# Optimization experiments

Hardware: AMD Instinct MI355X
Metric: run time of the kernel (lower is better)

The kernel has to match this reference:

```python
import jax, jax.numpy as jnp
import numpy as np

N_NODES = 100000
N_EDGES = 1600000
DIM = 64


def setup_inputs() -> dict:
    key = jax.random.key(0)
    ks = jax.random.split(key, 10)
    return {
        "h_real": jax.random.normal(ks[0], (N_NODES, DIM), dtype=jnp.float32),
        "h_imag": jax.random.normal(ks[1], (N_NODES, DIM), dtype=jnp.float32),
        "d": jax.random.uniform(ks[2], (N_NODES,), dtype=jnp.float32),
        "w_real": jax.random.normal(ks[3], (N_EDGES,), dtype=jnp.float32),
        "w_imag": jax.random.normal(ks[4], (N_EDGES,), dtype=jnp.float32),
        "src": jax.random.randint(ks[5], (N_EDGES,), 0, N_NODES, dtype=jnp.int32),
        "dst": jax.random.randint(ks[6], (N_EDGES,), 0, N_NODES, dtype=jnp.int32),
        "W1": jax.random.normal(ks[7], (DIM, DIM), dtype=jnp.float32) * (1.414 / np.sqrt(DIM)),
        "b1": jnp.zeros((DIM,), dtype=jnp.float32),
        "W2": jax.random.normal(ks[8], (DIM, DIM), dtype=jnp.float32) * (1.414 / np.sqrt(DIM)),
        "b2": jnp.zeros((DIM,), dtype=jnp.float32),
    }


def reference(h_real, h_imag, d, w_real, w_imag, src, dst, W1, b1, W2, b2):
    n = h_real.shape[0]
    # per-edge complex coefficient e = d_dst * d_src * (w_real + i w_imag)
    dd = d[dst] * d[src]                      # [E]
    e_r = (dd * w_real)[:, None]              # [E,1]
    e_i = (dd * w_imag)[:, None]              # [E,1]
    hr = h_real[src]                          # [E,D]
    hi = h_imag[src]                          # [E,D]
    # complex multiply e * h, fused single pass over edges
    m_r = e_r * hr - e_i * hi                 # [E,D]
    m_i = e_i * hr + e_r * hi                 # [E,D]
    z_real = jax.ops.segment_sum(m_r, dst, num_segments=n)  # [N,D]
    z_imag = jax.ops.segment_sum(m_i, dst, num_segments=n)  # [N,D]
    # note: original overwrites z_real first, then z_imag uses the NEW z_real
    zr = (z_real @ W1.T + b1) - (z_imag @ W2.T + b2)
    zi = (zr @ W2.T + b2) + (z_imag @ W1.T + b1)
    return zr, zi
```

## Files before the change

kernel.cpp:

```cpp
#include <hip/hip_runtime.h>
#include <hip/hip_bf16.h>

#define N_NODES 100000
#define N_EDGES 1600000
#define DIM 64

#define TILE 4096
#define B1 ((N_EDGES + TILE - 1) / TILE)
#define K1 ((N_NODES + 255) / 256)
#define NCOUNTS (K1 * B1)
#define SCAN_BLOCK 1024
#define NSB ((NCOUNTS + SCAN_BLOCK - 1) / SCAN_BLOCK)
#define PACKB ((N_NODES * DIM + 255) / 256)
#define PLACE_CAP 4736

typedef __attribute__((ext_vector_type(8))) short bf16x8;
typedef __attribute__((ext_vector_type(4))) float f32x4;

#if defined(__has_builtin)
#if __has_builtin(__builtin_amdgcn_fdot2_f32_bf16)
#define HAVE_DOT2 1
typedef __attribute__((ext_vector_type(2))) __bf16 bf16x2v;
#endif
#endif


__device__ __forceinline__ unsigned pack_bf16x2(float lo, float hi) {
  unsigned ulo = (unsigned)__hip_bfloat16_raw(__float2bfloat16(lo)).x;
  unsigned uhi = (unsigned)__hip_bfloat16_raw(__float2bfloat16(hi)).x;
  return ulo | (uhi << 16);
}
__device__ __forceinline__ float unpack_lo(unsigned u) {
  return __int_as_float((int)(u << 16));
}
__device__ __forceinline__ float unpack_hi(unsigned u) {
  return __int_as_float((int)(u & 0xFFFF0000u));
}
__device__ __forceinline__ unsigned short f2bf(float x) {
  return __hip_bfloat16_raw(__float2bfloat16(x)).x;
}

__global__ __launch_bounds__(256) void setup_fused_kernel(
    const float* __restrict__ h_real, const float* __restrict__ h_imag,
    unsigned* __restrict__ hpack, const float* __restrict__ W1,
    const float* __restrict__ b1, const float* __restrict__ W2,
    const float* __restrict__ b2, unsigned short* __restrict__ At,
    float* __restrict__ cvec, const int* __restrict__ dst,
    int* __restrict__ counts) {
  const int bid = blockIdx.x;
  const int tid = threadIdx.x;
  if (bid < PACKB) {
    const int i = bid * 256 + tid;
    if (i < N_NODES * DIM) hpack[i] = pack_bf16x2(h_real[i], h_imag[i]);
    return;
  }
  if (bid < PACKB + 64) {
    const int idx = (bid - PACKB) * 256 + tid;
    if (idx < 128 * 128) {
      const int n = idx >> 7, k = idx & 127;
      float v;
      if (n < 64) {
        v = (k < 64) ? W1[n * 64 + k] : -W2[n * 64 + (k - 64)];
      } else {
        const int nn = n - 64;
        if (k < 64) {
          float s = 0.0f;
          for (int j = 0; j < 64; ++j) s += W1[j * 64 + k] * W2[nn * 64 + j];
          v = s;
        } else {
          const int kk = k - 64;
          float s = 0.0f;
          for (int j = 0; j < 64; ++j) s += W2[j * 64 + kk] * W2[nn * 64 + j];
          v = W1[nn * 64 + kk] - s;
        }
      }
      At[n * 128 + k] = f2bf(v);
    }
    if (idx < 128) {
      if (idx < 64) {
        cvec[idx] = b1[idx] - b2[idx];
      } else {
        const int nn = idx - 64;
        float s = 0.0f;
        for (int j = 0; j < 64; ++j) s += (b1[j] - b2[j]) * W2[nn * 64 + j];
        cvec[idx] = s + b1[nn] + b2[nn];
      }
    }
    return;
  }
  __shared__ int lh[K1];
  const int hb = bid - PACKB - 64;
  for (int i = tid; i < K1; i += 256) lh[i] = 0;
  __syncthreads();
  const int e0 = hb * TILE;
  const int e1 = min(e0 + TILE, N_EDGES);
  for (int e = e0 + tid; e < e1; e += 256) atomicAdd(&lh[dst[e] >> 8], 1);
  __syncthreads();
  for (int b = tid; b < K1; b += 256) counts[b * B1 + hb] = lh[b];
}

__global__ __launch_bounds__(SCAN_BLOCK) void scan1_kernel(
    int* __restrict__ cnt, int* __restrict__ bsum) {
  __shared__ int s[SCAN_BLOCK];
  const int tid = threadIdx.x;
  const int i = blockIdx.x * SCAN_BLOCK + tid;
  const int v = (i < NCOUNTS) ? cnt[i] : 0;
  s[tid] = v;
  __syncthreads();
#pragma unroll
  for (int off = 1; off < SCAN_BLOCK; off <<= 1) {
    int t = (tid >= off) ? s[tid - off] : 0;
    __syncthreads();
    s[tid] += t;
    __syncthreads();
  }
  if (i < NCOUNTS) cnt[i] = s[tid] - v;
  if (tid == SCAN_BLOCK - 1) bsum[blockIdx.x] = s[tid];
}

__global__ void scan2_kernel(const int* __restrict__ bsum, int* __restrict__ bpre) {
  if (threadIdx.x == 0 && blockIdx.x == 0) {
    int run = 0;
    for (int b = 0; b < NSB; ++b) {
      bpre[b] = run;
      run += bsum[b];
    }
  }
}

__global__ __launch_bounds__(SCAN_BLOCK) void scan3_kernel(
    int* __restrict__ cnt, const int* __restrict__ bpre) {
  const int i = blockIdx.x * SCAN_BLOCK + threadIdx.x;
  if (i < NCOUNTS) cnt[i] += bpre[blockIdx.x];
}

__global__ __launch_bounds__(512) void partition_kernel(
    const int* __restrict__ src, const int* __restrict__ dst,
    const float* __restrict__ dvec,
    const float* __restrict__ w_real, const float* __restrict__ w_imag,
    const int* __restrict__ coffs, unsigned long long* __restrict__ records) {
  __shared__ unsigned long long stage[TILE];
  __shared__ unsigned short sb[TILE];
  __shared__ int lhist[512];
  __shared__ int lbase[K1];
  __shared__ int lcur[K1];
  __shared__ int gbase[K1];
  const int tid = threadIdx.x;
  const int blk = blockIdx.x;
  const int e0 = blk * TILE;
  const int cnt_t = min(TILE, N_EDGES - e0);

  lhist[tid] = 0;
  __syncthreads();
  for (int j = tid; j < cnt_t; j += 512) atomicAdd(&lhist[dst[e0 + j] >> 8], 1);
  __syncthreads();
  const int myc = lhist[tid];
  __syncthreads();
#pragma unroll
  for (int off = 1; off < 512; off <<= 1) {
    int v = (tid >= off) ? lhist[tid - off] : 0;
    __syncthreads();
    lhist[tid] += v;
    __syncthreads();
  }
  if (tid < K1) {
    const int ex = lhist[tid] - myc;
    lbase[tid] = ex;
    lcur[tid] = ex;
    gbase[tid] = coffs[tid * B1 + blk];
  }
  __syncthreads();

  for (int j = tid; j < cnt_t; j += 512) {
    const int e = e0 + j;
    const int t = dst[e];
    const int s = src[e];
    const int b = t >> 8;
    const float ds = dvec[s];
    const unsigned lo = (unsigned)s | ((unsigned)(t & 255) << 17);
    const unsigned hi = pack_bf16x2(ds * w_real[e], ds * w_imag[e]);
    const int r = atomicAdd(&lcur[b], 1);
    stage[r] = ((unsigned long long)hi << 32) | lo;
    sb[r] = (unsigned short)b;
  }
  __syncthreads();
  for (int i = tid; i < cnt_t; i += 512) {
    const int b = sb[i];
    records[gbase[b] + (i - lbase[b])] = stage[i];
  }
}

__global__ __launch_bounds__(256) void place_kernel(
    unsigned long long* __restrict__ records, const int* __restrict__ coffs,
    int* __restrict__ inc) {
  const int b = blockIdx.x;
  const int tid = threadIdx.x;
  const int bstart = coffs[b * B1];
  const int bend = (b == K1 - 1) ? N_EDGES : coffs[(b + 1) * B1];
  const int cnt = min(bend - bstart, PLACE_CAP);
  const int nbase = b << 8;
  const int nn = min(256, N_NODES - nbase);

  __shared__ unsigned long long stage[PLACE_CAP];
  __shared__ int ncnt[256];
  __shared__ int ncur[256];

  ncnt[tid] = 0;
  __syncthreads();
  for (int i = tid; i < cnt; i += 256) {
    const unsigned long long rec = records[bstart + i];
    stage[i] = rec;
    atomicAdd(&ncnt[((unsigned)rec >> 17) & 255], 1);
  }
  __syncthreads();
  const int myc = ncnt[tid];
  __syncthreads();
#pragma unroll
  for (int off = 1; off < 256; off <<= 1) {
    int v = (tid >= off) ? ncnt[tid - off] : 0;
    __syncthreads();
    ncnt[tid] += v;
    __syncthreads();
  }
  const int base = bstart + ncnt[tid] - myc;
  ncur[tid] = base;
  if (tid < nn) inc[nbase + tid] = base + myc;
  __syncthreads();
  for (int i = tid; i < cnt; i += 256) {
    const unsigned long long rec = stage[i];
    const int pos = atomicAdd(&ncur[((unsigned)rec >> 17) & 255], 1);
    records[pos] = rec;
  }
}

__global__ __launch_bounds__(1024) void pull_fused_kernel(
    const uint2* __restrict__ records, const int* __restrict__ inc,
    const float* __restrict__ dvec, const unsigned* __restrict__ hpack,
    const unsigned short* __restrict__ At, const float* __restrict__ cvec,
    float* __restrict__ zr_out, float* __restrict__ zi_out) {
  __shared__ __align__(16) unsigned short zs[16][136];
  const int lane = threadIdx.x & 63;
  const int wave = threadIdx.x >> 6;
  const int q4 = lane >> 4;
  const int m16 = lane & 15;
  const int node0 = blockIdx.x * 16;
  const int n = node0 + wave;

  const int start = (n == 0) ? 0 : inc[n - 1];
  const int end = inc[n];
  const int deg = end - start;
  const unsigned* __restrict__ hb = hpack + 4 * m16;

  float sr0 = 0.f, sr1 = 0.f, sr2 = 0.f, sr3 = 0.f;
  float si0 = 0.f, si1 = 0.f, si2 = 0.f, si3 = 0.f;

#if HAVE_DOT2
#define DOT2(acc, w, h)                                                     \
  acc = __builtin_amdgcn_fdot2_f32_bf16(__builtin_bit_cast(bf16x2v, (w)),   \
                                        __builtin_bit_cast(bf16x2v, (h)),   \
                                        acc, false)
#else
#define DOT2(acc, w, h)                                                     \
  {                                                                         \
    const float _wl = unpack_lo(w), _wh = unpack_hi(w);                     \
    const float _hl = unpack_lo(h), _hh = unpack_hi(h);                     \
    acc += _wl * _hl + _wh * _hh;                                           \
  }
#endif

#define ACC4(RR)                                                            \
  {                                                                         \
    const unsigned wneg = (RR).y ^ 0x80000000u;                             \
    const unsigned wswp = ((RR).y >> 16) | ((RR).y << 16);                  \
    const uint4 hv = *reinterpret_cast<const uint4*>(                       \
        hb + (size_t)((RR).x & 0x1FFFF) * DIM);                             \
    DOT2(sr0, wneg, hv.x); DOT2(si0, wswp, hv.x);                           \
    DOT2(sr1, wneg, hv.y); DOT2(si1, wswp, hv.y);                           \
    DOT2(sr2, wneg, hv.z); DOT2(si2, wswp, hv.z);                           \
    DOT2(sr3, wneg, hv.w); DOT2(si3, wswp, hv.w);                           \
  }

  int p = start + q4;
  const int nfull = deg >> 2;
  int i = 0;
  for (; i + 2 <= nfull; i += 2) {
    const uint2 r0 = records[p];
    const uint2 r1 = records[p + 4];
    ACC4(r0);
    ACC4(r1);
    p += 8;
  }
  if (i < nfull) {
    const uint2 r0 = records[p];
    ACC4(r0);
    p += 4;
  }
  if (p < end) {
    const uint2 r0 = records[p];
    ACC4(r0);
  }
#undef ACC4
#undef DOT2

#define QRED(v)                  \
  v += __shfl_xor(v, 16);        \
  v += __shfl_xor(v, 32);
  QRED(sr0) QRED(sr1) QRED(sr2) QRED(sr3)
  QRED(si0) QRED(si1) QRED(si2) QRED(si3)
#undef QRED

  const float dn = dvec[n];
  if (lane < 16) {
    uint2 rv, iv;
    rv.x = pack_bf16x2(dn * sr0, dn * sr1);
    rv.y = pack_bf16x2(dn * sr2, dn * sr3);
    iv.x = pack_bf16x2(dn * si0, dn * si1);
    iv.y = pack_bf16x2(dn * si2, dn * si3);
    *reinterpret_cast<uint2*>(&zs[wave][4 * lane]) = rv;
    *reinterpret_cast<uint2*>(&zs[wave][64 + 4 * lane]) = iv;
  }
  __syncthreads();

  if (wave < 8) {
    const int t = wave;
    const int m = lane & 15;
    const int q = lane >> 4;

    bf16x8 a[4];
#pragma unroll
    for (int c = 0; c < 4; ++c)
      a[c] = *reinterpret_cast<const bf16x8*>(&zs[m][c * 32 + q * 8]);

    f32x4 acc = (f32x4){0.f, 0.f, 0.f, 0.f};
    const unsigned short* brow = At + (size_t)(t * 16 + m) * 128 + q * 8;
#pragma unroll
    for (int c = 0; c < 4; ++c) {
      bf16x8 bfrag = *reinterpret_cast<const bf16x8*>(brow + c * 32);
      acc = __builtin_amdgcn_mfma_f32_16x16x32_bf16(a[c], bfrag, acc, 0, 0, 0);
    }

    const int nf = t * 16 + m;
    const float bias = cvec[nf];
    float* outp = (nf < 64) ? zr_out : zi_out;
    const int nn = nf & 63;
#pragma unroll
    for (int r = 0; r < 4; ++r) {
      const int node = node0 + q * 4 + r;
      outp[(size_t)node * 64 + nn] = acc[r] + bias;
    }
  }
}

extern "C" void kernel_launch(void* const* d_in, const int* in_sizes, int n_in,
                              void* d_out, int out_size, void* d_ws, size_t ws_size,
                              hipStream_t stream) {
  const float* h_real = (const float*)d_in[0];
  const float* h_imag = (const float*)d_in[1];
  const float* dvec   = (const float*)d_in[2];
  const float* w_real = (const float*)d_in[3];
  const float* w_imag = (const float*)d_in[4];
  const int*   src    = (const int*)d_in[5];
  const int*   dst    = (const int*)d_in[6];
  const float* W1     = (const float*)d_in[7];
  const float* b1     = (const float*)d_in[8];
  const float* W2     = (const float*)d_in[9];
  const float* b2     = (const float*)d_in[10];

  char* ws = (char*)d_ws;
  unsigned short* At = (unsigned short*)ws;
  float* cvec = (float*)(ws + 128 * 128 * 2);
  unsigned long long* records = (unsigned long long*)(ws + 33792);
  unsigned* hpack = (unsigned*)(ws + 33792 + (size_t)N_EDGES * 8);
  int* counts = (int*)(ws + 33792 + (size_t)N_EDGES * 8 + (size_t)N_NODES * DIM * 4);
  int* bsum = counts + NCOUNTS;
  int* bpre = bsum + NSB;
  int* inc  = bpre + NSB;

  float* zr_out = (float*)d_out;
  float* zi_out = zr_out + (size_t)N_NODES * DIM;

  setup_fused_kernel<<<PACKB + 64 + B1, 256, 0, stream>>>(
      h_real, h_imag, (unsigned*)hpack, W1, b1, W2, b2, At, cvec, dst, counts);
  scan1_kernel<<<NSB, SCAN_BLOCK, 0, stream>>>(counts, bsum);
  scan2_kernel<<<1, 64, 0, stream>>>(bsum, bpre);
  scan3_kernel<<<NSB, SCAN_BLOCK, 0, stream>>>(counts, bpre);
  partition_kernel<<<B1, 512, 0, stream>>>(src, dst, dvec, w_real, w_imag,
                                           counts, records);
  place_kernel<<<K1, 256, 0, stream>>>(records, counts, inc);
  pull_fused_kernel<<<N_NODES / 16, 1024, 0, stream>>>(
      (const uint2*)records, inc, dvec, hpack, At, cvec, zr_out, zi_out);
}
```

Before: 277.7 us.

## Replace two-level bucket partition with per-node atomic counting sort

Builds the CSR by counting edges per destination node with global atomics, scanning the 100k node counts with wave-shuffle scans, and scattering each record straight to its final slot through an atomic cursor. This drops the tile-bucket partition and place passes and their block-wide LDS staging. The pull kernel now has each 256-thread block handle 32 nodes, 8 per wave, and runs 4 MFMA tiles per wave; the h pack is vectorized to float4 loads. The cost is heavy global atomic contention in the histogram and scatter, scattered 8-byte record writes, and edge order within a node that now varies from run to run.

```diff
diff --git a/kernel.cpp b/kernel.cpp
--- a/kernel.cpp
+++ b/kernel.cpp
@@ -5,14 +5,12 @@
 #define N_EDGES 1600000
 #define DIM 64
 
-#define TILE 4096
-#define B1 ((N_EDGES + TILE - 1) / TILE)
-#define K1 ((N_NODES + 255) / 256)
-#define NCOUNTS (K1 * B1)
 #define SCAN_BLOCK 1024
-#define NSB ((NCOUNTS + SCAN_BLOCK - 1) / SCAN_BLOCK)
-#define PACKB ((N_NODES * DIM + 255) / 256)
-#define PLACE_CAP 4736
+#define NSB2 ((N_NODES + SCAN_BLOCK - 1) / SCAN_BLOCK)
+#define PACKB4 ((N_NODES * DIM / 4 + 255) / 256)
+#define HISTB ((N_EDGES / 4 + 255) / 256)
+#define NPW 8
+#define PULLB (N_NODES / 32)
 
 typedef __attribute__((ext_vector_type(8))) short bf16x8;
 typedef __attribute__((ext_vector_type(4))) float f32x4;
@@ -46,16 +44,23 @@
     const float* __restrict__ b1, const float* __restrict__ W2,
     const float* __restrict__ b2, unsigned short* __restrict__ At,
     float* __restrict__ cvec, const int* __restrict__ dst,
-    int* __restrict__ counts) {
+    int* __restrict__ cnt) {
   const int bid = blockIdx.x;
   const int tid = threadIdx.x;
-  if (bid < PACKB) {
+  if (bid < PACKB4) {
     const int i = bid * 256 + tid;
-    if (i < N_NODES * DIM) hpack[i] = pack_bf16x2(h_real[i], h_imag[i]);
+    const float4 hr = ((const float4*)h_real)[i];
+    const float4 hi = ((const float4*)h_imag)[i];
+    uint4 o;
+    o.x = pack_bf16x2(hr.x, hi.x);
+    o.y = pack_bf16x2(hr.y, hi.y);
+    o.z = pack_bf16x2(hr.z, hi.z);
+    o.w = pack_bf16x2(hr.w, hi.w);
+    ((uint4*)hpack)[i] = o;
     return;
   }
-  if (bid < PACKB + 64) {
-    const int idx = (bid - PACKB) * 256 + tid;
+  if (bid < PACKB4 + 64) {
+    const int idx = (bid - PACKB4) * 256 + tid;
     if (idx < 128 * 128) {
       const int n = idx >> 7, k = idx & 127;
       float v;
@@ -88,182 +93,133 @@
     }
     return;
   }
-  __shared__ int lh[K1];
-  const int hb = bid - PACKB - 64;
-  for (int i = tid; i < K1; i += 256) lh[i] = 0;
-  __syncthreads();
-  const int e0 = hb * TILE;
-  const int e1 = min(e0 + TILE, N_EDGES);
-  for (int e = e0 + tid; e < e1; e += 256) atomicAdd(&lh[dst[e] >> 8], 1);
-  __syncthreads();
-  for (int b = tid; b < K1; b += 256) counts[b * B1 + hb] = lh[b];
+  const int hb = bid - PACKB4 - 64;
+  const int e0 = (hb * 256 + tid) * 4;
+  if (e0 < N_EDGES) {
+    const int4 t4 = *(const int4*)(dst + e0);
+    atomicAdd(&cnt[t4.x], 1);
+    atomicAdd(&cnt[t4.y], 1);
+    atomicAdd(&cnt[t4.z], 1);
+    atomicAdd(&cnt[t4.w], 1);
+  }
 }
 
 __global__ __launch_bounds__(SCAN_BLOCK) void scan1_kernel(
     int* __restrict__ cnt, int* __restrict__ bsum) {
-  __shared__ int s[SCAN_BLOCK];
+  __shared__ int wsum[16];
   const int tid = threadIdx.x;
+  const int lane = tid & 63;
+  const int w = tid >> 6;
   const int i = blockIdx.x * SCAN_BLOCK + tid;
-  const int v = (i < NCOUNTS) ? cnt[i] : 0;
-  s[tid] = v;
-  __syncthreads();
-#pragma unroll
-  for (int off = 1; off < SCAN_BLOCK; off <<= 1) {
-    int t = (tid >= off) ? s[tid - off] : 0;
-    __syncthreads();
-    s[tid] += t;
-    __syncthreads();
-  }
-  if (i < NCOUNTS) cnt[i] = s[tid] - v;
-  if (tid == SCAN_BLOCK - 1) bsum[blockIdx.x] = s[tid];
-}
-
-__global__ void scan2_kernel(const int* __restrict__ bsum, int* __restrict__ bpre) {
-  if (threadIdx.x == 0 && blockIdx.x == 0) {
-    int run = 0;
-    for (int b = 0; b < NSB; ++b) {
-      bpre[b] = run;
-      run += bsum[b];
-    }
-  }
+  const int orig = (i < N_NODES) ? cnt[i] : 0;
+  int v = orig;
+#pragma unroll
+  for (int off = 1; off < 64; off <<= 1) {
+    int t = __shfl_up(v, off);
+    if (lane >= off) v += t;
+  }
+  if (lane == 63) wsum[w] = v;
+  __syncthreads();
+  if (w == 0) {
+    int s = (lane < 16) ? wsum[lane] : 0;
+#pragma unroll
+    for (int off = 1; off < 16; off <<= 1) {
+      int t = __shfl_up(s, off);
+      if (lane >= off) s += t;
+    }
+    if (lane < 16) wsum[lane] = s;
+  }
+  __syncthreads();
+  const int wex = (w == 0) ? 0 : wsum[w - 1];
+  if (i < N_NODES) cnt[i] = wex + v - orig;
+  if (tid == SCAN_BLOCK - 1) bsum[blockIdx.x] = wex + v;
+}
+
+__global__ __launch_bounds__(256) void scan2_kernel(
+    const int* __restrict__ bsum, int* __restrict__ bpre) {
+  __shared__ int wsum[4];
+  const int tid = threadIdx.x;
+  const int lane = tid & 63;
+  const int w = tid >> 6;
+  const int orig = (tid < NSB2) ? bsum[tid] : 0;
+  int v = orig;
+#pragma unroll
+  for (int off = 1; off < 64; off <<= 1) {
+    int t = __shfl_up(v, off);
+    if (lane >= off) v += t;
+  }
+  if (lane == 63) wsum[w] = v;
+  __syncthreads();
+  if (w == 0) {
+    int s = (lane < 4) ? wsum[lane] : 0;
+#pragma unroll
+    for (int off = 1; off < 4; off <<= 1) {
+      int t = __shfl_up(s, off);
+      if (lane >= off) s += t;
+    }
+    if (lane < 4) wsum[lane] = s;
+  }
+  __syncthreads();
+  const int wex = (w == 0) ? 0 : wsum[w - 1];
+  if (tid < NSB2) bpre[tid] = wex + v - orig;
 }
 
 __global__ __launch_bounds__(SCAN_BLOCK) void scan3_kernel(
-    int* __restrict__ cnt, const int* __restrict__ bpre) {
+    const int* __restrict__ cnt, const int* __restrict__ bpre,
+    int* __restrict__ cursor) {
   const int i = blockIdx.x * SCAN_BLOCK + threadIdx.x;
-  if (i < NCOUNTS) cnt[i] += bpre[blockIdx.x];
-}
-
-__global__ __launch_bounds__(512) void partition_kernel(
+  if (i < N_NODES) cursor[i] = cnt[i] + bpre[blockIdx.x];
+}
+
+__global__ __launch_bounds__(256) void scatter_kernel(
     const int* __restrict__ src, const int* __restrict__ dst,
     const float* __restrict__ dvec,
     const float* __restrict__ w_real, const float* __restrict__ w_imag,
-    const int* __restrict__ coffs, unsigned long long* __restrict__ records) {
-  __shared__ unsigned long long stage[TILE];
-  __shared__ unsigned short sb[TILE];
-  __shared__ int lhist[512];
-  __shared__ int lbase[K1];
-  __shared__ int lcur[K1];
-  __shared__ int gbase[K1];
-  const int tid = threadIdx.x;
-  const int blk = blockIdx.x;
-  const int e0 = blk * TILE;
-  const int cnt_t = min(TILE, N_EDGES - e0);
-
-  lhist[tid] = 0;
-  __syncthreads();
-  for (int j = tid; j < cnt_t; j += 512) atomicAdd(&lhist[dst[e0 + j] >> 8], 1);
-  __syncthreads();
-  const int myc = lhist[tid];
-  __syncthreads();
-#pragma unroll
-  for (int off = 1; off < 512; off <<= 1) {
-    int v = (tid >= off) ? lhist[tid - off] : 0;
-    __syncthreads();
-    lhist[tid] += v;
-    __syncthreads();
-  }
-  if (tid < K1) {
-    const int ex = lhist[tid] - myc;
-    lbase[tid] = ex;
-    lcur[tid] = ex;
-    gbase[tid] = coffs[tid * B1 + blk];
-  }
-  __syncthreads();
-
-  for (int j = tid; j < cnt_t; j += 512) {
-    const int e = e0 + j;
-    const int t = dst[e];
-    const int s = src[e];
-    const int b = t >> 8;
-    const float ds = dvec[s];
-    const unsigned lo = (unsigned)s | ((unsigned)(t & 255) << 17);
-    const unsigned hi = pack_bf16x2(ds * w_real[e], ds * w_imag[e]);
-    const int r = atomicAdd(&lcur[b], 1);
-    stage[r] = ((unsigned long long)hi << 32) | lo;
-    sb[r] = (unsigned short)b;
-  }
-  __syncthreads();
-  for (int i = tid; i < cnt_t; i += 512) {
-    const int b = sb[i];
-    records[gbase[b] + (i - lbase[b])] = stage[i];
-  }
-}
-
-__global__ __launch_bounds__(256) void place_kernel(
-    unsigned long long* __restrict__ records, const int* __restrict__ coffs,
-    int* __restrict__ inc) {
-  const int b = blockIdx.x;
-  const int tid = threadIdx.x;
-  const int bstart = coffs[b * B1];
-  const int bend = (b == K1 - 1) ? N_EDGES : coffs[(b + 1) * B1];
-  const int cnt = min(bend - bstart, PLACE_CAP);
-  const int nbase = b << 8;
-  const int nn = min(256, N_NODES - nbase);
-
-  __shared__ unsigned long long stage[PLACE_CAP];
-  __shared__ int ncnt[256];
-  __shared__ int ncur[256];
-
-  ncnt[tid] = 0;
-  __syncthreads();
-  for (int i = tid; i < cnt; i += 256) {
-    const unsigned long long rec = records[bstart + i];
-    stage[i] = rec;
-    atomicAdd(&ncnt[((unsigned)rec >> 17) & 255], 1);
-  }
-  __syncthreads();
-  const int myc = ncnt[tid];
-  __syncthreads();
-#pragma unroll
-  for (int off = 1; off < 256; off <<= 1) {
-    int v = (tid >= off) ? ncnt[tid - off] : 0;
-    __syncthreads();
-    ncnt[tid] += v;
-    __syncthreads();
-  }
-  const int base = bstart + ncnt[tid] - myc;
-  ncur[tid] = base;
-  if (tid < nn) inc[nbase + tid] = base + myc;
-  __syncthreads();
-  for (int i = tid; i < cnt; i += 256) {
-    const unsigned long long rec = stage[i];
-    const int pos = atomicAdd(&ncur[((unsigned)rec >> 17) & 255], 1);
-    records[pos] = rec;
-  }
-}
-
-__global__ __launch_bounds__(1024) void pull_fused_kernel(
+    int* __restrict__ cursor, unsigned long long* __restrict__ records) {
+  const int e0 = (blockIdx.x * 256 + threadIdx.x) * 4;
+  if (e0 >= N_EDGES) return;
+  const int4 s4 = *(const int4*)(src + e0);
+  const int4 t4 = *(const int4*)(dst + e0);
+  const float4 wr = *(const float4*)(w_real + e0);
+  const float4 wi = *(const float4*)(w_imag + e0);
+#define SCAT(SS, TT, WR, WI)                                              \
+  {                                                                       \
+    const float ds = dvec[SS];                                            \
+    const unsigned hi = pack_bf16x2(ds * (WR), ds * (WI));                \
+    const int pos = atomicAdd(&cursor[TT], 1);                            \
+    records[pos] = ((unsigned long long)hi << 32) | (unsigned)(SS);       \
+  }
+  SCAT(s4.x, t4.x, wr.x, wi.x)
+  SCAT(s4.y, t4.y, wr.y, wi.y)
+  SCAT(s4.z, t4.z, wr.z, wi.z)
+  SCAT(s4.w, t4.w, wr.w, wi.w)
+#undef SCAT
+}
+
+__global__ __launch_bounds__(256, 8) void pull_fused_kernel(
     const uint2* __restrict__ records, const int* __restrict__ inc,
     const float* __restrict__ dvec, const unsigned* __restrict__ hpack,
     const unsigned short* __restrict__ At, const float* __restrict__ cvec,
     float* __restrict__ zr_out, float* __restrict__ zi_out) {
-  __shared__ __align__(16) unsigned short zs[16][136];
-  const int lane = threadIdx.x & 63;
-  const int wave = threadIdx.x >> 6;
+  __shared__ __align__(16) unsigned short zs[32][136];
+  const int tid = threadIdx.x;
+  const int lane = tid & 63;
+  const int wave = tid >> 6;
   const int q4 = lane >> 4;
   const int m16 = lane & 15;
-  const int node0 = blockIdx.x * 16;
-  const int n = node0 + wave;
-
-  const int start = (n == 0) ? 0 : inc[n - 1];
-  const int end = inc[n];
-  const int deg = end - start;
+  const int node0 = blockIdx.x * 32;
   const unsigned* __restrict__ hb = hpack + 4 * m16;
 
-  float sr0 = 0.f, sr1 = 0.f, sr2 = 0.f, sr3 = 0.f;
-  float si0 = 0.f, si1 = 0.f, si2 = 0.f, si3 = 0.f;
-
 #if HAVE_DOT2
-#define DOT2(acc, w, h)                                                     \
-  acc = __builtin_amdgcn_fdot2_f32_bf16(__builtin_bit_cast(bf16x2v, (w)),   \
-                                        __builtin_bit_cast(bf16x2v, (h)),   \
+#define DOT2(acc, w_, h_)                                                   \
+  acc = __builtin_amdgcn_fdot2_f32_bf16(__builtin_bit_cast(bf16x2v, (w_)),  \
+                                        __builtin_bit_cast(bf16x2v, (h_)),  \
                                         acc, false)
 #else
-#define DOT2(acc, w, h)                                                     \
+#define DOT2(acc, w_, h_)                                                   \
   {                                                                         \
-    const float _wl = unpack_lo(w), _wh = unpack_hi(w);                     \
-    const float _hl = unpack_lo(h), _hh = unpack_hi(h);                     \
+    const float _wl = unpack_lo(w_), _wh = unpack_hi(w_);                   \
+    const float _hl = unpack_lo(h_), _hh = unpack_hi(h_);                   \
     acc += _wl * _hl + _wh * _hh;                                           \
   }
 #endif
@@ -273,80 +229,96 @@
     const unsigned wneg = (RR).y ^ 0x80000000u;                             \
     const unsigned wswp = ((RR).y >> 16) | ((RR).y << 16);                  \
     const uint4 hv = *reinterpret_cast<const uint4*>(                       \
-        hb + (size_t)((RR).x & 0x1FFFF) * DIM);                             \
+        hb + (size_t)(RR).x * DIM);                                         \
     DOT2(sr0, wneg, hv.x); DOT2(si0, wswp, hv.x);                           \
     DOT2(sr1, wneg, hv.y); DOT2(si1, wswp, hv.y);                           \
     DOT2(sr2, wneg, hv.z); DOT2(si2, wswp, hv.z);                           \
     DOT2(sr3, wneg, hv.w); DOT2(si3, wswp, hv.w);                           \
   }
 
-  int p = start + q4;
-  const int nfull = deg >> 2;
-  int i = 0;
-  for (; i + 2 <= nfull; i += 2) {
-    const uint2 r0 = records[p];
-    const uint2 r1 = records[p + 4];
-    ACC4(r0);
-    ACC4(r1);
-    p += 8;
-  }
-  if (i < nfull) {
-    const uint2 r0 = records[p];
-    ACC4(r0);
-    p += 4;
-  }
-  if (p < end) {
-    const uint2 r0 = records[p];
-    ACC4(r0);
+  for (int j = 0; j < NPW; ++j) {
+    const int n = node0 + wave * NPW + j;
+    const int start = (n == 0) ? 0 : inc[n - 1];
+    const int end = inc[n];
+    const int deg = end - start;
+
+    float sr0 = 0.f, sr1 = 0.f, sr2 = 0.f, sr3 = 0.f;
+    float si0 = 0.f, si1 = 0.f, si2 = 0.f, si3 = 0.f;
+
+    int p = start + q4;
+    const int nfull = deg >> 2;
+    int i = 0;
+    for (; i + 2 <= nfull; i += 2) {
+      const uint2 r0 = records[p];
+      const uint2 r1 = records[p + 4];
+      ACC4(r0);
+      ACC4(r1);
+      p += 8;
+    }
+    if (i < nfull) {
+      const uint2 r0 = records[p];
+      ACC4(r0);
+      p += 4;
+    }
+    if (p < end) {
+      const uint2 r0 = records[p];
+      ACC4(r0);
+    }
+
+#define QRED(v)                  \
+    v += __shfl_xor(v, 16);      \
+    v += __shfl_xor(v, 32);
+    QRED(sr0) QRED(sr1) QRED(sr2) QRED(sr3)
+    QRED(si0) QRED(si1) QRED(si2) QRED(si3)
+#undef QRED
+
+    const float dn = dvec[n];
+    if (lane < 16) {
+      const int zl = wave * NPW + j;
+      uint2 rv, iv;
+      rv.x = pack_bf16x2(dn * sr0, dn * sr1);
+      rv.y = pack_bf16x2(dn * sr2, dn * sr3);
+      iv.x = pack_bf16x2(dn * si0, dn * si1);
+      iv.y = pack_bf16x2(dn * si2, dn * si3);
+      *reinterpret_cast<uint2*>(&zs[zl][4 * lane]) = rv;
+      *reinterpret_cast<uint2*>(&zs[zl][64 + 4 * lane]) = iv;
+    }
   }
 #undef ACC4
 #undef DOT2
-
-#define QRED(v)                  \
-  v += __shfl_xor(v, 16);        \
-  v += __shfl_xor(v, 32);
-  QRED(sr0) QRED(sr1) QRED(sr2) QRED(sr3)
-  QRED(si0) QRED(si1) QRED(si2) QRED(si3)
-#undef QRED
-
-  const float dn = dvec[n];
-  if (lane < 16) {
-    uint2 rv, iv;
-    rv.x = pack_bf16x2(dn * sr0, dn * sr1);
-    rv.y = pack_bf16x2(dn * sr2, dn * sr3);
-    iv.x = pack_bf16x2(dn * si0, dn * si1);
-    iv.y = pack_bf16x2(dn * si2, dn * si3);
-    *reinterpret_cast<uint2*>(&zs[wave][4 * lane]) = rv;
-    *reinterpret_cast<uint2*>(&zs[wave][64 + 4 * lane]) = iv;
-  }
-  __syncthreads();
-
-  if (wave < 8) {
-    const int t = wave;
+  __syncthreads();
+
+  {
     const int m = lane & 15;
     const int q = lane >> 4;
-
-    bf16x8 a[4];
-#pragma unroll
-    for (int c = 0; c < 4; ++c)
-      a[c] = *reinterpret_cast<const bf16x8*>(&zs[m][c * 32 + q * 8]);
-
-    f32x4 acc = (f32x4){0.f, 0.f, 0.f, 0.f};
-    const unsigned short* brow = At + (size_t)(t * 16 + m) * 128 + q * 8;
-#pragma unroll
-    for (int c = 0; c < 4; ++c) {
-      bf16x8 bfrag = *reinterpret_cast<const bf16x8*>(brow + c * 32);
-      acc = __builtin_amdgcn_mfma_f32_16x16x32_bf16(a[c], bfrag, acc, 0, 0, 0);
-    }
-
-    const int nf = t * 16 + m;
-    const float bias = cvec[nf];
-    float* outp = (nf < 64) ? zr_out : zi_out;
-    const int nn = nf & 63;
-#pragma unroll
-    for (int r = 0; r < 4; ++r) {
-      const int node = node0 + q * 4 + r;
-      outp[(size_t)node * 64 + nn] = acc[r] + bias;
+#pragma unroll
+    for (int kk = 0; kk < 4; ++kk) {
+      const int tt = wave + kk * 4;
+      const int nh = tt >> 3;
+      const int ft = tt & 7;
+
+      bf16x8 a[4];
+#pragma unroll
+      for (int c = 0; c < 4; ++c)
+        a[c] = *reinterpret_cast<const bf16x8*>(&zs[nh * 16 + m][c * 32 + q * 8]);
+
+      f32x4 acc = (f32x4){0.f, 0.f, 0.f, 0.f};
+      const unsigned short* brow = At + (size_t)(ft * 16 + m) * 128 + q * 8;
+#pragma unroll
+      for (int c = 0; c < 4; ++c) {
+        bf16x8 bfrag = *reinterpret_cast<const bf16x8*>(brow + c * 32);
+        acc = __builtin_amdgcn_mfma_f32_16x16x32_bf16(a[c], bfrag, acc, 0, 0, 0);
+      }
+
+      const int nf = ft * 16 + m;
+      const float bias = cvec[nf];
+      float* outp = (nf < 64) ? zr_out : zi_out;
+      const int nnn = nf & 63;
+#pragma unroll
+      for (int r = 0; r < 4; ++r) {
+        const int node = node0 + nh * 16 + q * 4 + r;
+        outp[(size_t)node * 64 + nnn] = acc[r] + bias;
+      }
     }
   }
 }
@@ -371,22 +343,22 @@
   float* cvec = (float*)(ws + 128 * 128 * 2);
   unsigned long long* records = (unsigned long long*)(ws + 33792);
   unsigned* hpack = (unsigned*)(ws + 33792 + (size_t)N_EDGES * 8);
-  int* counts = (int*)(ws + 33792 + (size_t)N_EDGES * 8 + (size_t)N_NODES * DIM * 4);
-  int* bsum = counts + NCOUNTS;
-  int* bpre = bsum + NSB;
-  int* inc  = bpre + NSB;
+  int* cnt = (int*)(ws + 33792 + (size_t)N_EDGES * 8 + (size_t)N_NODES * DIM * 4);
+  int* bsum = cnt + N_NODES;
+  int* bpre = bsum + 128;
+  int* cursor = bpre + 128;
 
   float* zr_out = (float*)d_out;
   float* zi_out = zr_out + (size_t)N_NODES * DIM;
 
-  setup_fused_kernel<<<PACKB + 64 + B1, 256, 0, stream>>>(
-      h_real, h_imag, (unsigned*)hpack, W1, b1, W2, b2, At, cvec, dst, counts);
-  scan1_kernel<<<NSB, SCAN_BLOCK, 0, stream>>>(counts, bsum);
-  scan2_kernel<<<1, 64, 0, stream>>>(bsum, bpre);
-  scan3_kernel<<<NSB, SCAN_BLOCK, 0, stream>>>(counts, bpre);
-  partition_kernel<<<B1, 512, 0, stream>>>(src, dst, dvec, w_real, w_imag,
-                                           counts, records);
-  place_kernel<<<K1, 256, 0, stream>>>(records, counts, inc);
-  pull_fused_kernel<<<N_NODES / 16, 1024, 0, stream>>>(
-      (const uint2*)records, inc, dvec, hpack, At, cvec, zr_out, zi_out);
-}
+  hipMemsetAsync(cnt, 0, (size_t)N_NODES * sizeof(int), stream);
+  setup_fused_kernel<<<PACKB4 + 64 + HISTB, 256, 0, stream>>>(
+      h_real, h_imag, (unsigned*)hpack, W1, b1, W2, b2, At, cvec, dst, cnt);
+  scan1_kernel<<<NSB2, SCAN_BLOCK, 0, stream>>>(cnt, bsum);
+  scan2_kernel<<<1, 256, 0, stream>>>(bsum, bpre);
+  scan3_kernel<<<NSB2, SCAN_BLOCK, 0, stream>>>(cnt, bpre, cursor);
+  scatter_kernel<<<HISTB, 256, 0, stream>>>(src, dst, dvec, w_real, w_imag,
+                                            cursor, records);
+  pull_fused_kernel<<<PULLB, 256, 0, stream>>>(
+      (const uint2*)records, cursor, dvec, hpack, At, cvec, zr_out, zi_out);
+}
```

Result: slower. 382.3 us (+37.7%).
